# Kernel tuning notes

Measured on AMD Instinct MI355X. Metric: run time of the kernel, lower is better.

Reference implementation:

```python
import jax, jax.numpy as jnp
import numpy as np

NUM_SEQS = 128
TOTAL_TOKENS = 65536
HIDDEN = 768
FF = 3072
EPS = 1e-12  # torch F.normalize default eps


def _make_prompt_lens(rng: np.random.Generator) -> np.ndarray:
    # Ragged lengths in [64, 960], adjusted so they sum exactly to TOTAL_TOKENS.
    lens = rng.integers(64, 960, size=NUM_SEQS).astype(np.int64)
    lens = np.maximum(1, (lens * (TOTAL_TOKENS / lens.sum())).astype(np.int64))
    lens[-1] += TOTAL_TOKENS - lens.sum()
    assert lens.sum() == TOTAL_TOKENS and (lens > 0).all()
    return lens


def setup_inputs() -> dict:
    key = jax.random.key(0)
    k1, k2, k3 = jax.random.split(key, 3)
    hidden_states = jax.random.normal(k1, (TOTAL_TOKENS, HIDDEN), dtype=jnp.float32)
    prompt_lens = jnp.asarray(_make_prompt_lens(np.random.default_rng(0)))
    W1 = jax.random.normal(k2, (FF, HIDDEN), dtype=jnp.float32) * (HIDDEN ** -0.5)
    W2 = jax.random.normal(k3, (HIDDEN, FF), dtype=jnp.float32) * (FF ** -0.5)
    return {"hidden_states": hidden_states, "prompt_lens": prompt_lens, "W1": W1, "W2": W2}


def reference(hidden_states, prompt_lens, W1, W2):
    # hidden_states: [T, H]; prompt_lens: [S] summing to T.
    T = hidden_states.shape[0]
    S = prompt_lens.shape[0]
    # segment id of each token: index of first cumsum strictly greater than position
    seg_ids = jnp.searchsorted(jnp.cumsum(prompt_lens), jnp.arange(T), side="right")
    sums = jax.ops.segment_sum(hidden_states, seg_ids, num_segments=S)  # [S, H]
    pooled = sums / prompt_lens[:, None].astype(hidden_states.dtype)     # mean pool
    h = jnp.einsum("sh,fh->sf", pooled, W1)   # dense1: 768 -> 3072 (no bias)
    h = jnp.einsum("sf,hf->sh", h, W2)        # dense2: 3072 -> 768 (no bias)
    norm = jnp.linalg.norm(h, ord=2, axis=-1, keepdims=True)
    return h / jnp.maximum(norm, EPS)         # L2 normalize, [S, H]
```

## Files before the change

### kernel.cpp

```cpp
#include <hip/hip_runtime.h>

#define TOK   65536
#define HID   768
#define NSEQ  128
#define FFD   3072
#define CHUNK 64
#define NCHUNK (TOK / CHUNK)
#define KS1 5
#define KS2 20
#define KCH 160

__device__ __forceinline__ void add4(float4& a, const float4 b) {
  a.x += b.x; a.y += b.y; a.z += b.z; a.w += b.w;
}

__global__ __launch_bounds__(256) void prep_kernel(
    const int* __restrict__ lens, int* __restrict__ incl,
    int* __restrict__ start_seg) {
  __shared__ int sc[NSEQ];
  const int t = threadIdx.x;
  if (t < NSEQ) sc[t] = lens[t];
  __syncthreads();
  for (int off = 1; off < NSEQ; off <<= 1) {
    int v = 0;
    if (t < NSEQ && t >= off) v = sc[t - off];
    __syncthreads();
    if (t < NSEQ) sc[t] += v;
    __syncthreads();
  }
  if (t < NSEQ) incl[t] = sc[t];
  for (int c = t; c < NCHUNK; c += 256) {
    const int t0 = c * CHUNK;
    int lo = 0, hi = NSEQ - 1;
    while (lo < hi) { int mid = (lo + hi) >> 1; if (sc[mid] <= t0) lo = mid + 1; else hi = mid; }
    start_seg[c] = lo;
  }
}

__global__ __launch_bounds__(192) void pool_kernel(
    const float* __restrict__ x, const int* __restrict__ lens,
    const int* __restrict__ incl, const int* __restrict__ start_seg,
    float* __restrict__ pooled) {
  const int t0 = blockIdx.x * CHUNK;
  const int t1 = t0 + CHUNK;
  const int col = threadIdx.x;

  int seg = start_seg[blockIdx.x];
  int L = lens[seg];
  int cum = incl[seg] - L;

  const float4* xv = (const float4*)x + col;
  int t = t0;
  while (t < t1) {
    const int seg_end = cum + L;
    const int run_end = seg_end < t1 ? seg_end : t1;
    const int n = run_end - t;
    const float4* p = xv + (size_t)t * (HID / 4);
    float4 a0 = make_float4(0.f,0.f,0.f,0.f), a1 = a0, a2 = a0, a3 = a0;
    int i = 0;
    for (; i + 4 <= n; i += 4) {
      add4(a0, p[(size_t)(i+0) * (HID/4)]);
      add4(a1, p[(size_t)(i+1) * (HID/4)]);
      add4(a2, p[(size_t)(i+2) * (HID/4)]);
      add4(a3, p[(size_t)(i+3) * (HID/4)]);
    }
    for (; i < n; ++i) add4(a0, p[(size_t)i * (HID/4)]);
    add4(a0, a1); add4(a2, a3); add4(a0, a2);

    const float inv = 1.0f / (float)L;
    float* dst = pooled + (size_t)seg * HID + col * 4;
    atomicAdd(dst + 0, a0.x * inv);
    atomicAdd(dst + 1, a0.y * inv);
    atomicAdd(dst + 2, a0.z * inv);
    atomicAdd(dst + 3, a0.w * inv);

    t = run_end;
    if (run_end == seg_end) {
      cum = seg_end; ++seg;
      if (seg < NSEQ) L = lens[seg];
    }
  }
}

__global__ __launch_bounds__(256) void gemm_nt(
    const float* __restrict__ A, const float* __restrict__ B,
    float* __restrict__ Cp, int N, int Kt, int nsum, int pstride) {
  __shared__ float As[16][132];
  __shared__ float Bs[16][68];

  const int tid = threadIdx.x;
  const int f0 = blockIdx.x * 64;
  const int k0 = blockIdx.y * KCH;
  const int kend = (k0 + KCH) < Kt ? (k0 + KCH) : Kt;
  float* C = Cp + (size_t)blockIdx.y * NSEQ * N;
  const int fx = (tid & 15) * 4;
  const int sy = (tid >> 4) * 8;

  float acc[8][4];
  #pragma unroll
  for (int i = 0; i < 8; ++i)
    #pragma unroll
    for (int j = 0; j < 4; ++j) acc[i][j] = 0.f;

  for (int kc = k0; kc < kend; kc += 16) {
    #pragma unroll
    for (int r = 0; r < 2; ++r) {
      const int l = tid + 256 * r;
      const int s = l >> 2, k4 = (l & 3) * 4;
      const float* ap = A + (size_t)s * Kt + kc + k4;
      float4 v = *(const float4*)ap;
      for (int p = 1; p < nsum; ++p) {
        const float4 w = *(const float4*)(ap + (size_t)p * pstride);
        add4(v, w);
      }
      As[k4 + 0][s] = v.x; As[k4 + 1][s] = v.y;
      As[k4 + 2][s] = v.z; As[k4 + 3][s] = v.w;
    }
    {
      const int f = tid >> 2, k4 = (tid & 3) * 4;
      const float4 v = *(const float4*)(B + (size_t)(f0 + f) * Kt + kc + k4);
      Bs[k4 + 0][f] = v.x; Bs[k4 + 1][f] = v.y;
      Bs[k4 + 2][f] = v.z; Bs[k4 + 3][f] = v.w;
    }
    __syncthreads();
    #pragma unroll
    for (int kk = 0; kk < 16; ++kk) {
      const float4 aA = *(const float4*)&As[kk][sy];
      const float4 aB = *(const float4*)&As[kk][sy + 4];
      const float4 bb = *(const float4*)&Bs[kk][fx];
      acc[0][0] += aA.x*bb.x; acc[0][1] += aA.x*bb.y; acc[0][2] += aA.x*bb.z; acc[0][3] += aA.x*bb.w;
      acc[1][0] += aA.y*bb.x; acc[1][1] += aA.y*bb.y; acc[1][2] += aA.y*bb.z; acc[1][3] += aA.y*bb.w;
      acc[2][0] += aA.z*bb.x; acc[2][1] += aA.z*bb.y; acc[2][2] += aA.z*bb.z; acc[2][3] += aA.z*bb.w;
      acc[3][0] += aA.w*bb.x; acc[3][1] += aA.w*bb.y; acc[3][2] += aA.w*bb.z; acc[3][3] += aA.w*bb.w;
      acc[4][0] += aB.x*bb.x; acc[4][1] += aB.x*bb.y; acc[4][2] += aB.x*bb.z; acc[4][3] += aB.x*bb.w;
      acc[5][0] += aB.y*bb.x; acc[5][1] += aB.y*bb.y; acc[5][2] += aB.y*bb.z; acc[5][3] += aB.y*bb.w;
      acc[6][0] += aB.z*bb.x; acc[6][1] += aB.z*bb.y; acc[6][2] += aB.z*bb.z; acc[6][3] += aB.z*bb.w;
      acc[7][0] += aB.w*bb.x; acc[7][1] += aB.w*bb.y; acc[7][2] += aB.w*bb.z; acc[7][3] += aB.w*bb.w;
    }
    __syncthreads();
  }
  #pragma unroll
  for (int i = 0; i < 8; ++i) {
    float4 o = make_float4(acc[i][0], acc[i][1], acc[i][2], acc[i][3]);
    *(float4*)(C + (size_t)(sy + i) * N + f0 + fx) = o;
  }
}

__global__ __launch_bounds__(256) void norm_kernel(
    const float* __restrict__ outp, float* __restrict__ out) {
  const int s = blockIdx.x;
  const int tid = threadIdx.x;
  float v[3];
  #pragma unroll
  for (int j = 0; j < 3; ++j) {
    const int c = tid + 256 * j;
    float a = 0.f;
    for (int p = 0; p < KS2; ++p)
      a += outp[((size_t)p * NSEQ + s) * HID + c];
    v[j] = a;
  }
  float ss = v[0]*v[0] + v[1]*v[1] + v[2]*v[2];
  #pragma unroll
  for (int off = 32; off > 0; off >>= 1) ss += __shfl_down(ss, off, 64);
  __shared__ float wsum[4];
  if ((tid & 63) == 0) wsum[tid >> 6] = ss;
  __syncthreads();
  const float tot = wsum[0] + wsum[1] + wsum[2] + wsum[3];
  const float scale = 1.0f / fmaxf(sqrtf(tot), 1e-12f);
  #pragma unroll
  for (int j = 0; j < 3; ++j) out[(size_t)s * HID + tid + 256 * j] = v[j] * scale;
}

extern "C" void kernel_launch(void* const* d_in, const int* in_sizes, int n_in,
                              void* d_out, int out_size, void* d_ws, size_t ws_size,
                              hipStream_t stream) {
  const float* x    = (const float*)d_in[0];
  const int*   lens = (const int*)d_in[1];
  const float* W1   = (const float*)d_in[2];
  const float* W2   = (const float*)d_in[3];
  float* out = (float*)d_out;

  float* pooled = (float*)d_ws;
  float* h1p    = pooled + NSEQ * HID;
  float* outp   = h1p + (size_t)KS1 * NSEQ * FFD;
  int*   incl   = (int*)(outp + (size_t)KS2 * NSEQ * HID);
  int*   start_seg = incl + NSEQ;

  hipMemsetAsync(pooled, 0, (size_t)NSEQ * HID * sizeof(float), stream);

  prep_kernel<<<1, 256, 0, stream>>>(lens, incl, start_seg);
  pool_kernel<<<NCHUNK, 192, 0, stream>>>(x, lens, incl, start_seg, pooled);
  gemm_nt<<<dim3(FFD / 64, KS1), 256, 0, stream>>>(pooled, W1, h1p, FFD, HID, 1, 0);
  gemm_nt<<<dim3(HID / 64, KS2), 256, 0, stream>>>(h1p, W2, outp, HID, FFD, KS1, NSEQ * FFD);
  norm_kernel<<<NSEQ, 256, 0, stream>>>(outp, out);
}
```

Baseline: 355.1 us.

## Fuse prefix-scan into pooling, shrink GEMM tiles, add separate split-K reduction

The pool kernel now computes the length prefix sum and its own starting segment in each block, which removes the separate prep launch. It uses 32-token chunks and assumes a chunk spans at most two segments. The GEMM tile narrows to 32 columns with 4x4 per-thread accumulators, and the split-K factors change so more blocks run. The partial sums of the first GEMM are reduced by a new kernel instead of being re-summed inside the second GEMM's loads. The two-segment assumption holds here only because the minimum sequence length exceeds the chunk size, and the smaller tiles give less register reuse.

```diff
diff --git a/kernel.cpp b/kernel.cpp
--- a/kernel.cpp
+++ b/kernel.cpp
@@ -4,119 +4,104 @@
 #define HID   768
 #define NSEQ  128
 #define FFD   3072
-#define CHUNK 64
-#define NCHUNK (TOK / CHUNK)
-#define KS1 5
-#define KS2 20
-#define KCH 160
+#define PCH   32
+#define NPCH  (TOK / PCH)
+#define KS1   8
+#define KCH1  96
+#define KS2   24
+#define KCH2  128
 
 __device__ __forceinline__ void add4(float4& a, const float4 b) {
   a.x += b.x; a.y += b.y; a.z += b.z; a.w += b.w;
 }
 
-__global__ __launch_bounds__(256) void prep_kernel(
-    const int* __restrict__ lens, int* __restrict__ incl,
-    int* __restrict__ start_seg) {
+__global__ __launch_bounds__(192, 6) void pool_kernel(
+    const float* __restrict__ x, const int* __restrict__ lens,
+    float* __restrict__ pooled) {
   __shared__ int sc[NSEQ];
-  const int t = threadIdx.x;
-  if (t < NSEQ) sc[t] = lens[t];
+  const int tid = threadIdx.x;
+  if (tid < NSEQ) sc[tid] = lens[tid];
   __syncthreads();
   for (int off = 1; off < NSEQ; off <<= 1) {
     int v = 0;
-    if (t < NSEQ && t >= off) v = sc[t - off];
+    if (tid < NSEQ && tid >= off) v = sc[tid - off];
     __syncthreads();
-    if (t < NSEQ) sc[t] += v;
+    if (tid < NSEQ) sc[tid] += v;
     __syncthreads();
   }
-  if (t < NSEQ) incl[t] = sc[t];
-  for (int c = t; c < NCHUNK; c += 256) {
-    const int t0 = c * CHUNK;
-    int lo = 0, hi = NSEQ - 1;
-    while (lo < hi) { int mid = (lo + hi) >> 1; if (sc[mid] <= t0) lo = mid + 1; else hi = mid; }
-    start_seg[c] = lo;
-  }
-}
+  const int t0 = blockIdx.x * PCH;
+  int lo = 0, hi = NSEQ - 1;
+  while (lo < hi) { int mid = (lo + hi) >> 1; if (sc[mid] <= t0) lo = mid + 1; else hi = mid; }
+  const int seg = lo;
+  const int segend = sc[seg];
+  const int segstart = seg ? sc[seg - 1] : 0;
+  const float4* p = (const float4*)x + (size_t)t0 * (HID / 4) + tid;
 
-__global__ __launch_bounds__(192) void pool_kernel(
-    const float* __restrict__ x, const int* __restrict__ lens,
-    const int* __restrict__ incl, const int* __restrict__ start_seg,
-    float* __restrict__ pooled) {
-  const int t0 = blockIdx.x * CHUNK;
-  const int t1 = t0 + CHUNK;
-  const int col = threadIdx.x;
-
-  int seg = start_seg[blockIdx.x];
-  int L = lens[seg];
-  int cum = incl[seg] - L;
-
-  const float4* xv = (const float4*)x + col;
-  int t = t0;
-  while (t < t1) {
-    const int seg_end = cum + L;
-    const int run_end = seg_end < t1 ? seg_end : t1;
-    const int n = run_end - t;
-    const float4* p = xv + (size_t)t * (HID / 4);
+  if (segend >= t0 + PCH) {
     float4 a0 = make_float4(0.f,0.f,0.f,0.f), a1 = a0, a2 = a0, a3 = a0;
-    int i = 0;
-    for (; i + 4 <= n; i += 4) {
+    #pragma unroll
+    for (int i = 0; i < PCH; i += 4) {
       add4(a0, p[(size_t)(i+0) * (HID/4)]);
       add4(a1, p[(size_t)(i+1) * (HID/4)]);
       add4(a2, p[(size_t)(i+2) * (HID/4)]);
       add4(a3, p[(size_t)(i+3) * (HID/4)]);
     }
-    for (; i < n; ++i) add4(a0, p[(size_t)i * (HID/4)]);
     add4(a0, a1); add4(a2, a3); add4(a0, a2);
-
-    const float inv = 1.0f / (float)L;
-    float* dst = pooled + (size_t)seg * HID + col * 4;
+    const float inv = 1.0f / (float)(segend - segstart);
+    float* dst = pooled + (size_t)seg * HID + tid * 4;
     atomicAdd(dst + 0, a0.x * inv);
     atomicAdd(dst + 1, a0.y * inv);
     atomicAdd(dst + 2, a0.z * inv);
     atomicAdd(dst + 3, a0.w * inv);
-
-    t = run_end;
-    if (run_end == seg_end) {
-      cum = seg_end; ++seg;
-      if (seg < NSEQ) L = lens[seg];
-    }
+  } else {
+    const int n0 = segend - t0;
+    float4 a0 = make_float4(0.f,0.f,0.f,0.f), a1 = a0;
+    for (int i = 0; i < n0; ++i)  add4(a0, p[(size_t)i * (HID/4)]);
+    for (int i = n0; i < PCH; ++i) add4(a1, p[(size_t)i * (HID/4)]);
+    const float inv0 = 1.0f / (float)(segend - segstart);
+    const float inv1 = 1.0f / (float)(sc[seg + 1] - segend);
+    float* d0 = pooled + (size_t)seg * HID + tid * 4;
+    atomicAdd(d0 + 0, a0.x * inv0);
+    atomicAdd(d0 + 1, a0.y * inv0);
+    atomicAdd(d0 + 2, a0.z * inv0);
+    atomicAdd(d0 + 3, a0.w * inv0);
+    float* d1 = pooled + (size_t)(seg + 1) * HID + tid * 4;
+    atomicAdd(d1 + 0, a1.x * inv1);
+    atomicAdd(d1 + 1, a1.y * inv1);
+    atomicAdd(d1 + 2, a1.z * inv1);
+    atomicAdd(d1 + 3, a1.w * inv1);
   }
 }
 
 __global__ __launch_bounds__(256) void gemm_nt(
     const float* __restrict__ A, const float* __restrict__ B,
-    float* __restrict__ Cp, int N, int Kt, int nsum, int pstride) {
+    float* __restrict__ Cp, int N, int Kt, int kch) {
   __shared__ float As[16][132];
-  __shared__ float Bs[16][68];
+  __shared__ float Bs[16][36];
 
   const int tid = threadIdx.x;
-  const int f0 = blockIdx.x * 64;
-  const int k0 = blockIdx.y * KCH;
-  const int kend = (k0 + KCH) < Kt ? (k0 + KCH) : Kt;
+  const int f0 = blockIdx.x * 32;
+  const int k0 = blockIdx.y * kch;
   float* C = Cp + (size_t)blockIdx.y * NSEQ * N;
-  const int fx = (tid & 15) * 4;
-  const int sy = (tid >> 4) * 8;
+  const int fx = (tid & 7) * 4;
+  const int sy = (tid >> 3) * 4;
 
-  float acc[8][4];
+  float acc[4][4];
   #pragma unroll
-  for (int i = 0; i < 8; ++i)
+  for (int i = 0; i < 4; ++i)
     #pragma unroll
     for (int j = 0; j < 4; ++j) acc[i][j] = 0.f;
 
-  for (int kc = k0; kc < kend; kc += 16) {
+  for (int kc = k0; kc < k0 + kch; kc += 16) {
     #pragma unroll
     for (int r = 0; r < 2; ++r) {
       const int l = tid + 256 * r;
       const int s = l >> 2, k4 = (l & 3) * 4;
-      const float* ap = A + (size_t)s * Kt + kc + k4;
-      float4 v = *(const float4*)ap;
-      for (int p = 1; p < nsum; ++p) {
-        const float4 w = *(const float4*)(ap + (size_t)p * pstride);
-        add4(v, w);
-      }
+      const float4 v = *(const float4*)(A + (size_t)s * Kt + kc + k4);
       As[k4 + 0][s] = v.x; As[k4 + 1][s] = v.y;
       As[k4 + 2][s] = v.z; As[k4 + 3][s] = v.w;
     }
-    {
+    if (tid < 128) {
       const int f = tid >> 2, k4 = (tid & 3) * 4;
       const float4 v = *(const float4*)(B + (size_t)(f0 + f) * Kt + kc + k4);
       Bs[k4 + 0][f] = v.x; Bs[k4 + 1][f] = v.y;
@@ -125,25 +110,29 @@
     __syncthreads();
     #pragma unroll
     for (int kk = 0; kk < 16; ++kk) {
-      const float4 aA = *(const float4*)&As[kk][sy];
-      const float4 aB = *(const float4*)&As[kk][sy + 4];
+      const float4 aa = *(const float4*)&As[kk][sy];
       const float4 bb = *(const float4*)&Bs[kk][fx];
-      acc[0][0] += aA.x*bb.x; acc[0][1] += aA.x*bb.y; acc[0][2] += aA.x*bb.z; acc[0][3] += aA.x*bb.w;
-      acc[1][0] += aA.y*bb.x; acc[1][1] += aA.y*bb.y; acc[1][2] += aA.y*bb.z; acc[1][3] += aA.y*bb.w;
-      acc[2][0] += aA.z*bb.x; acc[2][1] += aA.z*bb.y; acc[2][2] += aA.z*bb.z; acc[2][3] += aA.z*bb.w;
-      acc[3][0] += aA.w*bb.x; acc[3][1] += aA.w*bb.y; acc[3][2] += aA.w*bb.z; acc[3][3] += aA.w*bb.w;
-      acc[4][0] += aB.x*bb.x; acc[4][1] += aB.x*bb.y; acc[4][2] += aB.x*bb.z; acc[4][3] += aB.x*bb.w;
-      acc[5][0] += aB.y*bb.x; acc[5][1] += aB.y*bb.y; acc[5][2] += aB.y*bb.z; acc[5][3] += aB.y*bb.w;
-      acc[6][0] += aB.z*bb.x; acc[6][1] += aB.z*bb.y; acc[6][2] += aB.z*bb.z; acc[6][3] += aB.z*bb.w;
-      acc[7][0] += aB.w*bb.x; acc[7][1] += aB.w*bb.y; acc[7][2] += aB.w*bb.z; acc[7][3] += aB.w*bb.w;
+      acc[0][0] += aa.x*bb.x; acc[0][1] += aa.x*bb.y; acc[0][2] += aa.x*bb.z; acc[0][3] += aa.x*bb.w;
+      acc[1][0] += aa.y*bb.x; acc[1][1] += aa.y*bb.y; acc[1][2] += aa.y*bb.z; acc[1][3] += aa.y*bb.w;
+      acc[2][0] += aa.z*bb.x; acc[2][1] += aa.z*bb.y; acc[2][2] += aa.z*bb.z; acc[2][3] += aa.z*bb.w;
+      acc[3][0] += aa.w*bb.x; acc[3][1] += aa.w*bb.y; acc[3][2] += aa.w*bb.z; acc[3][3] += aa.w*bb.w;
     }
     __syncthreads();
   }
   #pragma unroll
-  for (int i = 0; i < 8; ++i) {
-    float4 o = make_float4(acc[i][0], acc[i][1], acc[i][2], acc[i][3]);
-    *(float4*)(C + (size_t)(sy + i) * N + f0 + fx) = o;
-  }
+  for (int i = 0; i < 4; ++i)
+    *(float4*)(C + (size_t)(sy + i) * N + f0 + fx) =
+        make_float4(acc[i][0], acc[i][1], acc[i][2], acc[i][3]);
+}
+
+__global__ __launch_bounds__(256) void reduce_h1(
+    const float* __restrict__ h1p, float* __restrict__ h1) {
+  const size_t i = (size_t)blockIdx.x * 256 + threadIdx.x;
+  const float4* src = (const float4*)h1p;
+  float4 a = src[i];
+  #pragma unroll
+  for (int p = 1; p < KS1; ++p) add4(a, src[i + (size_t)p * (NSEQ * FFD / 4)]);
+  ((float4*)h1)[i] = a;
 }
 
 __global__ __launch_bounds__(256) void norm_kernel(
@@ -155,8 +144,7 @@
   for (int j = 0; j < 3; ++j) {
     const int c = tid + 256 * j;
     float a = 0.f;
-    for (int p = 0; p < KS2; ++p)
-      a += outp[((size_t)p * NSEQ + s) * HID + c];
+    for (int p = 0; p < KS2; ++p) a += outp[((size_t)p * NSEQ + s) * HID + c];
     v[j] = a;
   }
   float ss = v[0]*v[0] + v[1]*v[1] + v[2]*v[2];
@@ -182,15 +170,14 @@
 
   float* pooled = (float*)d_ws;
   float* h1p    = pooled + NSEQ * HID;
-  float* outp   = h1p + (size_t)KS1 * NSEQ * FFD;
-  int*   incl   = (int*)(outp + (size_t)KS2 * NSEQ * HID);
-  int*   start_seg = incl + NSEQ;
+  float* h1     = h1p + (size_t)KS1 * NSEQ * FFD;
+  float* outp   = h1 + NSEQ * FFD;
 
   hipMemsetAsync(pooled, 0, (size_t)NSEQ * HID * sizeof(float), stream);
 
-  prep_kernel<<<1, 256, 0, stream>>>(lens, incl, start_seg);
-  pool_kernel<<<NCHUNK, 192, 0, stream>>>(x, lens, incl, start_seg, pooled);
-  gemm_nt<<<dim3(FFD / 64, KS1), 256, 0, stream>>>(pooled, W1, h1p, FFD, HID, 1, 0);
-  gemm_nt<<<dim3(HID / 64, KS2), 256, 0, stream>>>(h1p, W2, outp, HID, FFD, KS1, NSEQ * FFD);
+  pool_kernel<<<NPCH, 192, 0, stream>>>(x, lens, pooled);
+  gemm_nt<<<dim3(FFD / 32, KS1), 256, 0, stream>>>(pooled, W1, h1p, FFD, HID, KCH1);
+  reduce_h1<<<NSEQ * FFD / 4 / 256, 256, 0, stream>>>(h1p, h1);
+  gemm_nt<<<dim3(HID / 32, KS2), 256, 0, stream>>>(h1, W2, outp, HID, FFD, KCH2);
   norm_kernel<<<NSEQ, 256, 0, stream>>>(outp, out);
 }
```

After: 338.7 us. 1.05x faster.
